# Kernel optimization log

Hardware: AMD Instinct MI355X
Metric: run time of the kernel (lower is better)

## Reference

```python
import jax, jax.numpy as jnp
import numpy as np

N_HEADS = 16
ROPE_THETA = 10000.0


def _rope_tables(seq_len, head_dim, dtype=jnp.float32):
    half = head_dim // 2
    inv_freq = 1.0 / (ROPE_THETA ** (jnp.arange(0, half, dtype=jnp.float32) / half))
    t = jnp.arange(seq_len, dtype=jnp.float32)
    freqs = jnp.outer(t, inv_freq)  # (S, half)
    return jnp.cos(freqs).astype(dtype), jnp.sin(freqs).astype(dtype)


def _apply_rope(x, cos, sin):
    # x: (B, H, S, hd); cos/sin: (S, hd//2)
    half = x.shape[-1] // 2
    x1, x2 = x[..., :half], x[..., half:]
    c = cos[None, None, :, :]
    s = sin[None, None, :, :]
    return jnp.concatenate([x1 * c - x2 * s, x1 * s + x2 * c], axis=-1)


def setup_inputs() -> dict:
    key = jax.random.key(0)
    k1, k2, k3 = jax.random.split(key, 3)
    B, S, D = 4, 2048, 2048
    hd = D // N_HEADS
    x = jax.random.normal(k1, (B, S, D), dtype=jnp.float32)
    cos, sin = _rope_tables(S, hd)
    w_qkv = jax.random.normal(k2, (D, 3 * D), dtype=jnp.float32) * (D ** -0.5)
    w_out = jax.random.normal(k3, (D, D), dtype=jnp.float32) * (D ** -0.5)
    return {"x": x, "cos": cos, "sin": sin, "w_qkv": w_qkv, "w_out": w_out}


def reference(x, cos, sin, w_qkv, w_out):
    B, S, D = x.shape
    H = N_HEADS
    hd = D // H
    qkv = x @ w_qkv  # (B, S, 3D)
    qkv = qkv.reshape(B, S, 3, H, hd).transpose(2, 0, 3, 1, 4)  # (3, B, H, S, hd)
    q, k, v = qkv[0], qkv[1], qkv[2]
    q = _apply_rope(q, cos, sin)
    k = _apply_rope(k, cos, sin)
    scale = 1.0 / jnp.sqrt(jnp.asarray(hd, dtype=x.dtype))
    scores = jnp.einsum('bhqd,bhkd->bhqk', q, k) * scale  # (B, H, S, S)
    causal = jnp.tril(jnp.ones((S, S), dtype=bool))
    scores = jnp.where(causal[None, None, :, :], scores, jnp.asarray(-1e30, dtype=scores.dtype))
    p = jax.nn.softmax(scores, axis=-1)
    out = jnp.einsum('bhqk,bhkd->bhqd', p, v)  # (B, H, S, hd)
    out = out.transpose(0, 2, 1, 3).reshape(B, S, D)
    return out @ w_out
```

## Files before the change

kernel.cpp:

```cpp
#include <hip/hip_runtime.h>
#include <hip/hip_bf16.h>
#include <stdint.h>

typedef __bf16  bf16x8  __attribute__((ext_vector_type(8)));
typedef float   floatx4 __attribute__((ext_vector_type(4)));

typedef __attribute__((address_space(1))) void gvoid_t;
typedef __attribute__((address_space(3))) void svoid_t;

__device__ __forceinline__ void gld16(ushort* lds, const ushort* g) {
  __builtin_amdgcn_global_load_lds((gvoid_t*)g, (svoid_t*)lds, 16, 0, 0);
}

__device__ __forceinline__ ushort f2bf(float f) {
  union { float f; unsigned u; } v; v.f = f;
  unsigned u = v.u;
  return (ushort)((u + 0x7fffu + ((u >> 16) & 1u)) >> 16);
}
__device__ __forceinline__ float bf2f(ushort h) {
  union { unsigned u; float f; } v; v.u = ((unsigned)h) << 16; return v.f;
}
__device__ __forceinline__ unsigned pk2bf(float a, float b) {
  __hip_bfloat162 h = __float22bfloat162_rn(make_float2(a, b));
  union { __hip_bfloat162 h; unsigned u; } v; v.h = h; return v.u;
}

__global__ __launch_bounds__(256) void cvt_f32_bf16(
    const float* __restrict__ in, ushort* __restrict__ out) {
  int i = blockIdx.x * 256 + threadIdx.x;
  float4 a = ((const float4*)in)[i];
  ushort4 o;
  o.x = f2bf(a.x); o.y = f2bf(a.y); o.z = f2bf(a.z); o.w = f2bf(a.w);
  ((ushort4*)out)[i] = o;
}

__global__ __launch_bounds__(256) void transpose_cvt(
    const float* __restrict__ in, ushort* __restrict__ out, int R, int C) {
  __shared__ ushort tile[64][65];
  const int r0 = blockIdx.y * 64, c0 = blockIdx.x * 64;
  const int t = threadIdx.x;
#pragma unroll
  for (int rep = 0; rep < 16; rep++) {
    int idx = rep * 256 + t;
    int r = idx >> 6, c = idx & 63;
    tile[r][c] = f2bf(in[(size_t)(r0 + r) * C + c0 + c]);
  }
  __syncthreads();
#pragma unroll
  for (int rep = 0; rep < 16; rep++) {
    int idx = rep * 256 + t;
    int r = idx >> 6, c = idx & 63;
    out[(size_t)(c0 + r) * R + r0 + c] = tile[c][r];
  }
}

template <int EPI>
__global__ __launch_bounds__(512, 1) void gemm256(
    const ushort* __restrict__ A, const ushort* __restrict__ Bt,
    float* __restrict__ Cf,
    ushort* __restrict__ C0, ushort* __restrict__ C1, ushort* __restrict__ C2,
    int M, int N, int K) {
  __shared__ __align__(16) ushort As[2][2][256 * 32];
  __shared__ __align__(16) ushort Bs[2][2][256 * 32];
  const int t = threadIdx.x;
  const int lane = t & 63;
  const int w = t >> 6;
  const int l15 = lane & 15;
  const int quad = lane >> 4;
  const int m0 = blockIdx.y * 256;
  const int n0 = blockIdx.x * 256;
  const int wmB = (w >> 2) * 128;
  const int wnB = (w & 3) * 64;

  const int cS = (lane & 3) ^ ((lane >> 3) & 3);
  const size_t aoff = (size_t)(m0 + w * 32 + (lane >> 2)) * K + cS * 8;
  const size_t boff = (size_t)(n0 + w * 32 + (lane >> 2)) * K + cS * 8;

  const ushort* const Ab = &As[0][0][0];
  const ushort* const Bb = &Bs[0][0][0];
  const ushort* aP[4];
  const ushort* bP[4];
#pragma unroll
  for (int m = 0; m < 4; ++m) {
    int r = wmB + m * 16 + l15;
    int c = quad ^ ((r >> 1) & 3);
    aP[m] = Ab + r * 32 + c * 8;
  }
#pragma unroll
  for (int n = 0; n < 4; ++n) {
    int r = wnB + n * 16 + l15;
    int c = quad ^ ((r >> 1) & 3);
    bP[n] = Bb + r * 32 + c * 8;
  }

#define STAGE_A(db, kh, tile)                                                \
  { size_t ko_ = (size_t)(tile) * 64 + (kh) * 32;                            \
    gld16(&As[db][kh][w * 1024],       A + aoff + ko_);                      \
    gld16(&As[db][kh][w * 1024 + 512], A + aoff + 16 * (size_t)K + ko_); }
#define STAGE_B(db, kh, tile)                                                \
  { size_t ko_ = (size_t)(tile) * 64 + (kh) * 32;                            \
    gld16(&Bs[db][kh][w * 1024],       Bt + boff + ko_);                     \
    gld16(&Bs[db][kh][w * 1024 + 512], Bt + boff + 16 * (size_t)K + ko_); }

#define LDA(AF, db, kh, mh)                                                  \
  _Pragma("unroll") for (int m_ = 0; m_ < 4; ++m_)                           \
    AF[m_] = *(const bf16x8*)(aP[m_] +                                       \
                              ((db) * 16384 + (kh) * 8192 + (mh) * 2048));
#define LDB(db, kh)                                                          \
  _Pragma("unroll") for (int n_ = 0; n_ < 4; ++n_)                           \
    bfr[n_] = *(const bf16x8*)(bP[n_] + ((db) * 16384 + (kh) * 8192));

  floatx4 acc[8][4];
  const floatx4 zero = {0.f, 0.f, 0.f, 0.f};
#pragma unroll
  for (int i = 0; i < 8; i++)
#pragma unroll
    for (int j = 0; j < 4; j++) acc[i][j] = zero;

  bf16x8 af0[4], af1[4], bfr[4];

#define PH(db, kh, mh, AFU, AFL, ndb, nkh, nmh, STAGE)                       \
  __builtin_amdgcn_s_barrier();                                              \
  if ((mh) == 0) { LDB(db, kh) }                                             \
  asm volatile("s_waitcnt lgkmcnt(0)" ::: "memory");                         \
  __builtin_amdgcn_sched_barrier(0);                                         \
  __builtin_amdgcn_s_setprio(1);                                             \
  _Pragma("unroll") for (int m_ = 0; m_ < 4; ++m_)                           \
    _Pragma("unroll") for (int n_ = 0; n_ < 4; ++n_)                         \
      acc[(mh) * 4 + m_][n_] = __builtin_amdgcn_mfma_f32_16x16x32_bf16(      \
          AFU[m_], bfr[n_], acc[(mh) * 4 + m_][n_], 0, 0, 0);                \
  __builtin_amdgcn_s_setprio(0);                                             \
  __builtin_amdgcn_sched_barrier(0);                                         \
  LDA(AFL, ndb, nkh, nmh)                                                    \
  STAGE                                                                      \
  asm volatile("s_waitcnt vmcnt(8)" ::: "memory");

  const int NT = K >> 6;
  const int NI = K >> 7;

  STAGE_A(0, 0, 0);
  STAGE_B(0, 0, 0);
  STAGE_A(0, 1, 0);
  STAGE_B(0, 1, 0);
  STAGE_A(1, 0, 1);
  STAGE_B(1, 0, 1);
  asm volatile("s_waitcnt vmcnt(4)" ::: "memory");
  __builtin_amdgcn_s_barrier();
  LDA(af0, 0, 0, 0)

  for (int i = 0; i < NI; ++i) {
    const int t1 = 2 * i + 1;
    int t2 = 2 * i + 2, t3 = 2 * i + 3;
    if (t2 > NT - 1) t2 = NT - 1;
    if (t3 > NT - 1) t3 = NT - 1;
    PH(0, 0, 0, af0, af1, 0, 0, 1, STAGE_A(1, 1, t1))
    PH(0, 0, 1, af1, af0, 0, 1, 0, STAGE_B(1, 1, t1))
    PH(0, 1, 0, af0, af1, 0, 1, 1, STAGE_A(0, 0, t2))
    PH(0, 1, 1, af1, af0, 1, 0, 0, STAGE_B(0, 0, t2))
    PH(1, 0, 0, af0, af1, 1, 0, 1, STAGE_A(0, 1, t2))
    PH(1, 0, 1, af1, af0, 1, 1, 0, STAGE_B(0, 1, t2))
    PH(1, 1, 0, af0, af1, 1, 1, 1, STAGE_A(1, 0, t3))
    PH(1, 1, 1, af1, af0, 0, 0, 0, STAGE_B(1, 0, t3))
  }
  asm volatile("s_waitcnt vmcnt(0)" ::: "memory");

#undef PH
#undef LDA
#undef LDB
#undef STAGE_A
#undef STAGE_B

  if (EPI == 0) {
#pragma unroll
    for (int m = 0; m < 8; ++m)
#pragma unroll
      for (int n = 0; n < 4; ++n)
#pragma unroll
        for (int r = 0; r < 4; ++r) {
          int row = m0 + wmB + m * 16 + quad * 4 + r;
          int col = n0 + wnB + n * 16 + l15;
          Cf[(size_t)row * N + col] = acc[m][n][r];
        }
  } else {
    const int colW = n0 + wnB;
    const int sel = colW >> 11;
    const int h = (colW >> 7) & 15;
    if (sel < 2) {
      ushort* dst = (sel == 0) ? C0 : C1;
#pragma unroll
      for (int m = 0; m < 8; ++m) {
        int rowb = m0 + wmB + m * 16 + quad * 4;
        int b = rowb >> 11, s = rowb & 2047;
#pragma unroll
        for (int n = 0; n < 4; ++n) {
          int d = (colW + n * 16 + l15) & 127;
#pragma unroll
          for (int r = 0; r < 4; ++r)
            dst[((size_t)(b * 16 + h) * 2048 + (s + r)) * 128 + d] =
                f2bf(acc[m][n][r]);
        }
      }
    } else {
#pragma unroll
      for (int m = 0; m < 8; ++m) {
        int rowb = m0 + wmB + m * 16 + quad * 4;
        int b = rowb >> 11, s = rowb & 2047;
#pragma unroll
        for (int n = 0; n < 4; ++n) {
          int d = (colW + n * 16 + l15) & 127;
          ushort4 pk;
          pk.x = f2bf(acc[m][n][0]);
          pk.y = f2bf(acc[m][n][1]);
          pk.z = f2bf(acc[m][n][2]);
          pk.w = f2bf(acc[m][n][3]);
          *(ushort4*)&C2[((size_t)(b * 16 + h) * 128 + d) * 2048 + s] = pk;
        }
      }
    }
  }
}

__global__ __launch_bounds__(256) void rope_kernel(
    ushort* __restrict__ Q, ushort* __restrict__ Kb,
    const float* __restrict__ cosT, const float* __restrict__ sinT) {
  unsigned gid = blockIdx.x * 256u + threadIdx.x;
  int d = gid & 63;
  int s = (gid >> 6) & 2047;
  int bh = (gid >> 17) & 63;
  const bool isK = (gid >> 23) != 0;
  ushort* buf = isK ? Kb : Q;
  const float sc = isK ? 1.0f
                       : 0.08838834764831845f * 1.4426950408889634f;
  size_t base = ((size_t)bh * 2048 + s) * 128;
  float x1 = bf2f(buf[base + d]);
  float x2 = bf2f(buf[base + d + 64]);
  float c = cosT[s * 64 + d];
  float sn = sinT[s * 64 + d];
  buf[base + d] = f2bf((x1 * c - x2 * sn) * sc);
  buf[base + d + 64] = f2bf((x1 * sn + x2 * c) * sc);
}

__global__ __launch_bounds__(256, 4) void attn_kernel(
    const ushort* __restrict__ Q, const ushort* __restrict__ Kb,
    const ushort* __restrict__ VT, ushort* __restrict__ O) {
  __shared__ __align__(16) ushort Ks[64 * 128];
  __shared__ __align__(16) ushort Vs[128 * 64];
  __shared__ __align__(16) ushort Ps[64 * 64];
  const int t = threadIdx.x, lane = t & 63, w = t >> 6;
  const int l15 = lane & 15, quad = lane >> 4;
  const int bid = blockIdx.x;
  const int tq = 31 - (bid >> 6);
  const int bh = bid & 63;
  const int q0 = tq * 64 + w * 16;
  const int qrow = q0 + l15;
  const size_t hbase = (size_t)bh * 2048 * 128;
  const float NEGINF = -__builtin_inff();

  bf16x8 aq[4];
#pragma unroll
  for (int kb = 0; kb < 4; kb++)
    aq[kb] = *(const bf16x8*)&Q[hbase + (size_t)qrow * 128 + kb * 32 + quad * 8];

  float m2 = NEGINF, lsum = 0.f;
  floatx4 oacc[8];
  const floatx4 zero = {0.f, 0.f, 0.f, 0.f};
#pragma unroll
  for (int dj = 0; dj < 8; dj++) oacc[dj] = zero;

  const int ntk = tq + 1;

  for (int tk = 0; tk < ntk; tk++) {
    __syncthreads();
#pragma unroll
    for (int it = 0; it < 4; it++) {
      int o = (w * 4 + it) * 64 + lane;
      {
        int row = o >> 4;
        int c = (o & 15) ^ (row & 15);
        gld16(&Ks[(w * 4 + it) * 512],
              Kb + hbase + (size_t)(tk * 64 + row) * 128 + c * 8);
      }
      {
        int row = o >> 3;
        int c = (o & 7) ^ (row & 7);
        gld16(&Vs[(w * 4 + it) * 512],
              VT + hbase + (size_t)row * 2048 + tk * 64 + c * 8);
      }
    }
    __syncthreads();

    floatx4 sacc[4];
#pragma unroll
    for (int j = 0; j < 4; j++) sacc[j] = zero;
#pragma unroll
    for (int kb = 0; kb < 4; kb++) {
#pragma unroll
      for (int j = 0; j < 4; j++) {
        int row = j * 16 + l15;
        int c = (kb * 4 + quad) ^ (row & 15);
        bf16x8 kf = *(const bf16x8*)&Ks[row * 128 + c * 8];
        sacc[j] = __builtin_amdgcn_mfma_f32_16x16x32_bf16(kf, aq[kb], sacc[j],
                                                          0, 0, 0);
      }
    }

    if (tk == tq) {
#pragma unroll
      for (int j = 0; j < 4; j++)
#pragma unroll
        for (int r = 0; r < 4; r++) {
          int kcol = tk * 64 + j * 16 + quad * 4 + r;
          if (kcol > qrow) sacc[j][r] = NEGINF;
        }
    }

    float mx = sacc[0][0];
#pragma unroll
    for (int j = 0; j < 4; j++)
#pragma unroll
      for (int r = 0; r < 4; r++) mx = fmaxf(mx, sacc[j][r]);
    mx = fmaxf(mx, __shfl_xor(mx, 16));
    mx = fmaxf(mx, __shfl_xor(mx, 32));
    float mnew = fmaxf(m2, mx);
    float alpha = __builtin_exp2f(m2 - mnew);
    m2 = mnew;
    float rs = 0.f;
#pragma unroll
    for (int j = 0; j < 4; j++)
#pragma unroll
      for (int r = 0; r < 4; r++) {
        float p = __builtin_exp2f(sacc[j][r] - mnew);
        sacc[j][r] = p;
        rs += p;
      }
    rs += __shfl_xor(rs, 16);
    rs += __shfl_xor(rs, 32);
    lsum = lsum * alpha + rs;
    if (__any(alpha < 1.0f)) {
#pragma unroll
      for (int dj = 0; dj < 8; dj++) oacc[dj] *= alpha;
    }

#pragma unroll
    for (int j = 0; j < 4; j++) {
      unsigned lo = pk2bf(sacc[j][0], sacc[j][1]);
      unsigned hi = pk2bf(sacc[j][2], sacc[j][3]);
      int g = j * 2 + (quad >> 1);
      int gp = g ^ (l15 & 7);
      uint2 pv; pv.x = lo; pv.y = hi;
      *(uint2*)&Ps[(w * 16 + l15) * 64 + gp * 8 + (quad & 1) * 4] = pv;
    }

    bf16x8 bp[2];
#pragma unroll
    for (int kk = 0; kk < 2; kk++) {
      int g = kk * 4 + quad;
      int gp = g ^ (l15 & 7);
      bp[kk] = *(const bf16x8*)&Ps[(w * 16 + l15) * 64 + gp * 8];
    }
#pragma unroll
    for (int kk = 0; kk < 2; kk++)
#pragma unroll
      for (int dj = 0; dj < 8; dj++) {
        int rowd = dj * 16 + l15;
        int c = (kk * 4 + quad) ^ (rowd & 7);
        bf16x8 av = *(const bf16x8*)&Vs[rowd * 64 + c * 8];
        oacc[dj] = __builtin_amdgcn_mfma_f32_16x16x32_bf16(av, bp[kk], oacc[dj],
                                                           0, 0, 0);
      }
  }

  const int b = bh >> 4, h = bh & 15;
  const float rl = 1.0f / lsum;
  const size_t obase = ((size_t)(b * 2048 + qrow)) * 2048 + h * 128;
#pragma unroll
  for (int dj = 0; dj < 8; dj++) {
    ushort4 pk;
    pk.x = f2bf(oacc[dj][0] * rl);
    pk.y = f2bf(oacc[dj][1] * rl);
    pk.z = f2bf(oacc[dj][2] * rl);
    pk.w = f2bf(oacc[dj][3] * rl);
    *(ushort4*)&O[obase + dj * 16 + quad * 4] = pk;
  }
}

extern "C" void kernel_launch(void* const* d_in, const int* in_sizes, int n_in,
                              void* d_out, int out_size, void* d_ws, size_t ws_size,
                              hipStream_t stream) {
  const float* x    = (const float*)d_in[0];
  const float* cosT = (const float*)d_in[1];
  const float* sinT = (const float*)d_in[2];
  const float* wqkv = (const float*)d_in[3];
  const float* wout = (const float*)d_in[4];
  float* out = (float*)d_out;
  char* ws = (char*)d_ws;

  ushort* xbf   = (ushort*)d_out;
  ushort* wqkvT = (ushort*)(ws);
  ushort* Ob    = (ushort*)(ws);
  ushort* woutT = (ushort*)(ws + 33554432);
  ushort* Qb    = (ushort*)(ws + 41943040);
  ushort* Kbuf  = (ushort*)(ws + 75497472);
  ushort* VTb   = (ushort*)(ws + 109051904);

  cvt_f32_bf16<<<16384, 256, 0, stream>>>(x, xbf);
  transpose_cvt<<<dim3(96, 32), 256, 0, stream>>>(wqkv, wqkvT, 2048, 6144);
  transpose_cvt<<<dim3(32, 32), 256, 0, stream>>>(wout, woutT, 2048, 2048);
  gemm256<1><<<dim3(24, 32), 512, 0, stream>>>(xbf, wqkvT, nullptr,
                                               Qb, Kbuf, VTb, 8192, 6144, 2048);
  rope_kernel<<<65536, 256, 0, stream>>>(Qb, Kbuf, cosT, sinT);
  attn_kernel<<<2048, 256, 0, stream>>>(Qb, Kbuf, VTb, Ob);
  gemm256<0><<<dim3(8, 32), 512, 0, stream>>>(Ob, woutT, out,
                                              nullptr, nullptr, nullptr,
                                              8192, 2048, 2048);
}
```

Measured before the change: 600.2 us.

## Double-buffer K/V tiles and use 128-row query blocks in attention

The attention kernel now uses 512 threads covering 128 query rows per block, so each K/V tile in LDS is shared by twice as many queries. It also double-buffers K and V in shared memory, issuing the async global-to-LDS loads for the next tile before computing on the current one, which drops one barrier per iteration. This targets global load latency and redundant K/V traffic. In exchange it doubles LDS use per block, which may reduce occupancy, and the last two tiles need causal masking.

```diff
diff --git a/kernel.cpp b/kernel.cpp
--- a/kernel.cpp
+++ b/kernel.cpp
@@ -240,21 +240,27 @@
   buf[base + d + 64] = f2bf((x1 * sn + x2 * c) * sc);
 }
 
-__global__ __launch_bounds__(256, 4) void attn_kernel(
+__global__ __launch_bounds__(512, 4) void attn_kernel(
     const ushort* __restrict__ Q, const ushort* __restrict__ Kb,
     const ushort* __restrict__ VT, ushort* __restrict__ O) {
-  __shared__ __align__(16) ushort Ks[64 * 128];
-  __shared__ __align__(16) ushort Vs[128 * 64];
-  __shared__ __align__(16) ushort Ps[64 * 64];
+  __shared__ __align__(16) ushort Ks[2][64 * 128];
+  __shared__ __align__(16) ushort Vs[2][128 * 64];
+  __shared__ __align__(16) ushort Ps[128 * 64];
   const int t = threadIdx.x, lane = t & 63, w = t >> 6;
   const int l15 = lane & 15, quad = lane >> 4;
   const int bid = blockIdx.x;
-  const int tq = 31 - (bid >> 6);
+  const int tq = 15 - (bid >> 6);
   const int bh = bid & 63;
-  const int q0 = tq * 64 + w * 16;
-  const int qrow = q0 + l15;
+  const int qrow = tq * 128 + w * 16 + l15;
   const size_t hbase = (size_t)bh * 2048 * 128;
   const float NEGINF = -__builtin_inff();
+
+  const int kr0 = w * 8 + quad, kr1 = w * 8 + 4 + quad;
+  const ushort* kS0 = Kb + hbase + (size_t)kr0 * 128 + (l15 ^ (kr0 & 15)) * 8;
+  const ushort* kS1 = Kb + hbase + (size_t)kr1 * 128 + (l15 ^ (kr1 & 15)) * 8;
+  const int vr0 = w * 16 + (lane >> 3), vr1 = w * 16 + 8 + (lane >> 3);
+  const ushort* vS0 = VT + hbase + (size_t)vr0 * 2048 + ((lane & 7) ^ (vr0 & 7)) * 8;
+  const ushort* vS1 = VT + hbase + (size_t)vr1 * 2048 + ((lane & 7) ^ (vr1 & 7)) * 8;
 
   bf16x8 aq[4];
 #pragma unroll
@@ -267,27 +273,23 @@
 #pragma unroll
   for (int dj = 0; dj < 8; dj++) oacc[dj] = zero;
 
-  const int ntk = tq + 1;
-
+  const int ntk = 2 * tq + 2;
+
+#define STAGE(b, tile)                                                \
+  { gld16(&Ks[b][(w * 2 + 0) * 512], kS0 + (size_t)(tile) * 8192);    \
+    gld16(&Ks[b][(w * 2 + 1) * 512], kS1 + (size_t)(tile) * 8192);    \
+    gld16(&Vs[b][(w * 2 + 0) * 512], vS0 + (size_t)(tile) * 64);      \
+    gld16(&Vs[b][(w * 2 + 1) * 512], vS1 + (size_t)(tile) * 64); }
+
+  STAGE(0, 0)
+  asm volatile("s_waitcnt vmcnt(0)" ::: "memory");
+  __builtin_amdgcn_s_barrier();
+
+  int cur = 0;
   for (int tk = 0; tk < ntk; tk++) {
-    __syncthreads();
-#pragma unroll
-    for (int it = 0; it < 4; it++) {
-      int o = (w * 4 + it) * 64 + lane;
-      {
-        int row = o >> 4;
-        int c = (o & 15) ^ (row & 15);
-        gld16(&Ks[(w * 4 + it) * 512],
-              Kb + hbase + (size_t)(tk * 64 + row) * 128 + c * 8);
-      }
-      {
-        int row = o >> 3;
-        int c = (o & 7) ^ (row & 7);
-        gld16(&Vs[(w * 4 + it) * 512],
-              VT + hbase + (size_t)row * 2048 + tk * 64 + c * 8);
-      }
-    }
-    __syncthreads();
+    if (tk + 1 < ntk) STAGE(cur ^ 1, tk + 1)
+    const ushort* Kc = &Ks[cur][0];
+    const ushort* Vc = &Vs[cur][0];
 
     floatx4 sacc[4];
 #pragma unroll
@@ -298,13 +300,13 @@
       for (int j = 0; j < 4; j++) {
         int row = j * 16 + l15;
         int c = (kb * 4 + quad) ^ (row & 15);
-        bf16x8 kf = *(const bf16x8*)&Ks[row * 128 + c * 8];
+        bf16x8 kf = *(const bf16x8*)&Kc[row * 128 + c * 8];
         sacc[j] = __builtin_amdgcn_mfma_f32_16x16x32_bf16(kf, aq[kb], sacc[j],
                                                           0, 0, 0);
       }
     }
 
-    if (tk == tq) {
+    if (tk >= ntk - 2) {
 #pragma unroll
       for (int j = 0; j < 4; j++)
 #pragma unroll
@@ -364,11 +366,16 @@
       for (int dj = 0; dj < 8; dj++) {
         int rowd = dj * 16 + l15;
         int c = (kk * 4 + quad) ^ (rowd & 7);
-        bf16x8 av = *(const bf16x8*)&Vs[rowd * 64 + c * 8];
+        bf16x8 av = *(const bf16x8*)&Vc[rowd * 64 + c * 8];
         oacc[dj] = __builtin_amdgcn_mfma_f32_16x16x32_bf16(av, bp[kk], oacc[dj],
                                                            0, 0, 0);
       }
-  }
+
+    asm volatile("s_waitcnt vmcnt(0)" ::: "memory");
+    __builtin_amdgcn_s_barrier();
+    cur ^= 1;
+  }
+#undef STAGE
 
   const int b = bh >> 4, h = bh & 15;
   const float rl = 1.0f / lsum;
@@ -409,7 +416,7 @@
   gemm256<1><<<dim3(24, 32), 512, 0, stream>>>(xbf, wqkvT, nullptr,
                                                Qb, Kbuf, VTb, 8192, 6144, 2048);
   rope_kernel<<<65536, 256, 0, stream>>>(Qb, Kbuf, cosT, sinT);
-  attn_kernel<<<2048, 256, 0, stream>>>(Qb, Kbuf, VTb, Ob);
+  attn_kernel<<<1024, 512, 0, stream>>>(Qb, Kbuf, VTb, Ob);
   gemm256<0><<<dim3(8, 32), 512, 0, stream>>>(Ob, woutT, out,
                                               nullptr, nullptr, nullptr,
                                               8192, 2048, 2048);
```

After: 587.5 us. -2.1%, faster.
